# Optimization experiments

Hardware: AMD Instinct MI355X
Metric: run time of the kernel (lower is better)

Reference implementation:

```python
import jax, jax.numpy as jnp
import numpy as np

GROUP_SIZE = 128
SCALE = 1.0 / np.sqrt(GROUP_SIZE)
LOG2_N = 7  # log2(128)


def _fwht(x):
    # x: (B, n) with n = GROUP_SIZE. Sylvester-ordered fast Walsh-Hadamard transform.
    B, n = x.shape
    h = 1
    for _ in range(LOG2_N):
        x = x.reshape(B, n // (2 * h), 2, h)
        a = x[:, :, 0, :]
        b = x[:, :, 1, :]
        x = jnp.stack([a + b, a - b], axis=2).reshape(B, n)
        h *= 2
    return x


def setup_inputs() -> dict:
    key = jax.random.key(0)
    x = jax.random.normal(key, (4, 4096, 4096), dtype=jnp.float32)
    return {"x": x}


def reference(x):
    x_shape = x.shape
    xg = x.reshape(-1, GROUP_SIZE)          # (B*S*H/128, 128)
    out = _fwht(xg) * jnp.asarray(SCALE, x.dtype)
    return out.reshape(x_shape)
```

## Files before the change

### kernel.cpp

```cpp
#include <hip/hip_runtime.h>


__global__ __launch_bounds__(256) void fwht128_kernel(const float* __restrict__ x,
                                                      float* __restrict__ out,
                                                      int n4) {
    int idx = blockIdx.x * blockDim.x + threadIdx.x;
    if (idx >= n4) return;

    const float4* __restrict__ in4 = (const float4*)x;
    float4* __restrict__ out4 = (float4*)out;

    float4 v = in4[idx];

    float a0 = v.x + v.y;
    float a1 = v.x - v.y;
    float a2 = v.z + v.w;
    float a3 = v.z - v.w;
    float r0 = a0 + a2;
    float r1 = a1 + a3;
    float r2 = a0 - a2;
    float r3 = a1 - a3;

    float r[4] = {r0, r1, r2, r3};

    const int lane = threadIdx.x & 63;

    #pragma unroll
    for (int m = 1; m <= 16; m <<= 1) {
        const bool upper = (lane & m) != 0;
        #pragma unroll
        for (int j = 0; j < 4; ++j) {
            float p = __shfl_xor(r[j], m, 64);
            r[j] = upper ? (p - r[j]) : (r[j] + p);
        }
    }

    constexpr float SCALE = 0.08838834764831845f;
    float4 o;
    o.x = r[0] * SCALE;
    o.y = r[1] * SCALE;
    o.z = r[2] * SCALE;
    o.w = r[3] * SCALE;
    out4[idx] = o;
}

extern "C" void kernel_launch(void* const* d_in, const int* in_sizes, int n_in,
                              void* d_out, int out_size, void* d_ws, size_t ws_size,
                              hipStream_t stream) {
    const float* x = (const float*)d_in[0];
    float* out = (float*)d_out;
    int n = in_sizes[0];
    int n4 = n >> 2;
    const int block = 256;
    int grid = (n4 + block - 1) / block;
    fwht128_kernel<<<grid, block, 0, stream>>>(x, out, n4);
}
```

Baseline: 411.1 us.

## Process 16 elements per thread with in-register butterflies and fewer shuffles

Each thread now loads four float4 vectors (16 contiguous elements), performs four in-register butterfly stages, and needs only three cross-lane shuffle stages across 8 lanes per 128-group. This cuts shuffle traffic per element and the thread count by four. The trade-off is strided per-instruction memory access across lanes, higher register use, and fewer waves to hide latency.

```diff
diff --git a/kernel.cpp b/kernel.cpp
--- a/kernel.cpp
+++ b/kernel.cpp
@@ -3,45 +3,56 @@
 
 __global__ __launch_bounds__(256) void fwht128_kernel(const float* __restrict__ x,
                                                       float* __restrict__ out,
-                                                      int n4) {
+                                                      int nthreads) {
     int idx = blockIdx.x * blockDim.x + threadIdx.x;
-    if (idx >= n4) return;
+    if (idx >= nthreads) return;
 
     const float4* __restrict__ in4 = (const float4*)x;
     float4* __restrict__ out4 = (float4*)out;
 
-    float4 v = in4[idx];
+    float4 v0 = in4[4 * idx + 0];
+    float4 v1 = in4[4 * idx + 1];
+    float4 v2 = in4[4 * idx + 2];
+    float4 v3 = in4[4 * idx + 3];
 
-    float a0 = v.x + v.y;
-    float a1 = v.x - v.y;
-    float a2 = v.z + v.w;
-    float a3 = v.z - v.w;
-    float r0 = a0 + a2;
-    float r1 = a1 + a3;
-    float r2 = a0 - a2;
-    float r3 = a1 - a3;
+    float r[16] = {v0.x, v0.y, v0.z, v0.w,
+                   v1.x, v1.y, v1.z, v1.w,
+                   v2.x, v2.y, v2.z, v2.w,
+                   v3.x, v3.y, v3.z, v3.w};
 
-    float r[4] = {r0, r1, r2, r3};
+    #pragma unroll
+    for (int h = 1; h <= 8; h <<= 1) {
+        #pragma unroll
+        for (int j = 0; j < 16; ++j) {
+            if (!(j & h)) {
+                float a = r[j];
+                float b = r[j ^ h];
+                r[j]     = a + b;
+                r[j ^ h] = a - b;
+            }
+        }
+    }
 
     const int lane = threadIdx.x & 63;
-
     #pragma unroll
-    for (int m = 1; m <= 16; m <<= 1) {
+    for (int m = 1; m <= 4; m <<= 1) {
         const bool upper = (lane & m) != 0;
         #pragma unroll
-        for (int j = 0; j < 4; ++j) {
+        for (int j = 0; j < 16; ++j) {
             float p = __shfl_xor(r[j], m, 64);
             r[j] = upper ? (p - r[j]) : (r[j] + p);
         }
     }
 
     constexpr float SCALE = 0.08838834764831845f;
-    float4 o;
-    o.x = r[0] * SCALE;
-    o.y = r[1] * SCALE;
-    o.z = r[2] * SCALE;
-    o.w = r[3] * SCALE;
-    out4[idx] = o;
+    float4 o0 = {r[0] * SCALE,  r[1] * SCALE,  r[2] * SCALE,  r[3] * SCALE};
+    float4 o1 = {r[4] * SCALE,  r[5] * SCALE,  r[6] * SCALE,  r[7] * SCALE};
+    float4 o2 = {r[8] * SCALE,  r[9] * SCALE,  r[10] * SCALE, r[11] * SCALE};
+    float4 o3 = {r[12] * SCALE, r[13] * SCALE, r[14] * SCALE, r[15] * SCALE};
+    out4[4 * idx + 0] = o0;
+    out4[4 * idx + 1] = o1;
+    out4[4 * idx + 2] = o2;
+    out4[4 * idx + 3] = o3;
 }
 
 extern "C" void kernel_launch(void* const* d_in, const int* in_sizes, int n_in,
@@ -50,8 +61,8 @@
     const float* x = (const float*)d_in[0];
     float* out = (float*)d_out;
     int n = in_sizes[0];
-    int n4 = n >> 2;
+    int nthreads = n >> 4;
     const int block = 256;
-    int grid = (n4 + block - 1) / block;
-    fwht128_kernel<<<grid, block, 0, stream>>>(x, out, n4);
+    int grid = (nthreads + block - 1) / block;
+    fwht128_kernel<<<grid, block, 0, stream>>>(x, out, nthreads);
 }
```

New measurement: 443.1 us. 7.8% more time.
